# Performance work log

Hardware: AMD Instinct MI355X
Metric: run time of the kernel (lower is better)

## Reference

```python
import jax, jax.numpy as jnp
import numpy as np

# Dims (match init_kwargs / input_specs)
B, S, HID = 1, 2048, 2048
NH, NKV, HD = 16, 4, 128          # head_dim = HID // NH
REP = NH // NKV                    # num_key_value_groups
BLOCK_SIZE, LOCAL_BLOCKS, SINK_NUM = 8, 4, 4
SCALING = HD ** -0.5


def rotate_half(x):
    x1, x2 = jnp.split(x, 2, axis=-1)
    return jnp.concatenate([-x2, x1], axis=-1)


def setup_inputs() -> dict:
    key = jax.random.key(0)
    ks = jax.random.split(key, 7)
    return {
        "hidden_states": jax.random.normal(ks[0], (B, S, HID), jnp.float32),
        "cos": jax.random.uniform(ks[1], (B, S, HD), jnp.float32, minval=-1.0, maxval=1.0),
        "sin": jax.random.uniform(ks[2], (B, S, HD), jnp.float32, minval=-1.0, maxval=1.0),
        # Projection weights stored as [in, out] so x @ W matches nn.Linear (bias=False).
        "Wq": 0.02 * jax.random.normal(ks[3], (HID, NH * HD), jnp.float32),
        "Wk": 0.02 * jax.random.normal(ks[4], (HID, NKV * HD), jnp.float32),
        "Wv": 0.02 * jax.random.normal(ks[5], (HID, NKV * HD), jnp.float32),
        "Wo": 0.02 * jax.random.normal(ks[6], (NH * HD, HID), jnp.float32),
    }


def sink_local_mask(seq_len):
    # query i attends to: sink tokens j < min(SINK_NUM, i), and local window
    # max(0, i - LOCAL_BLOCKS*BLOCK_SIZE) <= j <= i (diagonal included so every
    # row has at least one valid key; see notes).
    i = jnp.arange(seq_len)[:, None]
    j = jnp.arange(seq_len)[None, :]
    sink = j < jnp.minimum(SINK_NUM, i)
    local = (j >= i - LOCAL_BLOCKS * BLOCK_SIZE) & (j <= i)
    return sink | local  # [S, S] bool, broadcast over (B, H)


def reference(hidden_states, cos, sin, Wq, Wk, Wv, Wo):
    # projections -> [B, H, S, D]
    q = (hidden_states @ Wq).reshape(B, S, NH, HD).transpose(0, 2, 1, 3)
    k = (hidden_states @ Wk).reshape(B, S, NKV, HD).transpose(0, 2, 1, 3)
    v = (hidden_states @ Wv).reshape(B, S, NKV, HD).transpose(0, 2, 1, 3)
    # rotary embedding, cos/sin broadcast over head dim (unsqueeze_dim=1)
    c = cos[:, None, :, :]
    s = sin[:, None, :, :]
    q = q * c + rotate_half(q) * s
    k = k * c + rotate_half(k) * s
    # repeat_kv (GQA) -> [B, NH, S, D]
    k = jnp.repeat(k, REP, axis=1)
    v = jnp.repeat(v, REP, axis=1)
    # sink + local sparse attention (dense compute + mask, as in source)
    scores = jnp.einsum('bhqd,bhkd->bhqk', q, k) * SCALING
    mask = sink_local_mask(S)
    scores = jnp.where(mask, scores, -jnp.inf)
    attn_weights = jax.nn.softmax(scores, axis=-1)
    attn_output = jnp.einsum('bhqk,bhkd->bhqd', attn_weights, v)
    # Faithful to source: view(B, S, -1) on the [B, H, S, D] layout WITHOUT a
    # transpose(1,2) first (the original code omits it).
    attn_output = attn_output.reshape(B, S, NH * HD)
    attn_output = attn_output @ Wo
    return attn_output, attn_weights
```

## Files before the change

kernel.cpp:

```cpp
#include <hip/hip_runtime.h>

typedef unsigned short ushort_t;
typedef __attribute__((ext_vector_type(8))) short short8;
typedef __attribute__((ext_vector_type(4))) float f32x4;
typedef __attribute__((ext_vector_type(8))) unsigned short us8;
typedef __attribute__((ext_vector_type(4))) unsigned short us4;

#define SEQ 2048
#define HIDD 2048
#define XLD 3072
#define SCALING 0.08838834764831843f

__device__ __forceinline__ float bf2f(ushort_t u) {
    unsigned int x = ((unsigned int)u) << 16;
    return __builtin_bit_cast(float, x);
}
__device__ __forceinline__ ushort_t f2bf(float f) {
    unsigned int u = __builtin_bit_cast(unsigned int, f);
    u += 0x7fffu + ((u >> 16) & 1u);
    return (ushort_t)(u >> 16);
}

__device__ __forceinline__ void transpose_tile(
    const float* __restrict__ W, ushort_t* __restrict__ Wt,
    int N, int n0, int k0, int dstRow0) {
    __shared__ ushort_t t[64 * 80];
    const int tid = threadIdx.x;
    {
        const int kl = tid >> 4;
        const int nc = (tid & 15) * 4;
        #pragma unroll
        for (int p = 0; p < 4; ++p) {
            int k = kl + p * 16;
            float4 v = *(const float4*)(W + (size_t)(k0 + k) * N + n0 + nc);
            t[(nc + 0) * 80 + k] = f2bf(v.x);
            t[(nc + 1) * 80 + k] = f2bf(v.y);
            t[(nc + 2) * 80 + k] = f2bf(v.z);
            t[(nc + 3) * 80 + k] = f2bf(v.w);
        }
    }
    __syncthreads();
    {
        const int nl = tid >> 3;
        const int kc = (tid & 7) * 8;
        #pragma unroll
        for (int p = 0; p < 2; ++p) {
            int n = nl + p * 32;
            *(us8*)(Wt + (size_t)(dstRow0 + n) * HIDD + k0 + kc) =
                *(const us8*)&t[n * 80 + kc];
        }
    }
}

__global__ __launch_bounds__(256) void transpose_all(
    const float* __restrict__ Wq, const float* __restrict__ Wk,
    const float* __restrict__ Wv, const float* __restrict__ Wo,
    const float* __restrict__ hid,
    ushort_t* __restrict__ Wqkvt, ushort_t* __restrict__ Wot,
    ushort_t* __restrict__ Hb) {
    int bx = blockIdx.x, k0 = blockIdx.y * 64;
    if (bx < 32)       transpose_tile(Wq, Wqkvt, 2048, bx * 64,        k0, bx * 64);
    else if (bx < 40)  transpose_tile(Wk, Wqkvt, 512,  (bx - 32) * 64, k0, 2048 + (bx - 32) * 64);
    else if (bx < 48)  transpose_tile(Wv, Wqkvt, 512,  (bx - 40) * 64, k0, 2560 + (bx - 40) * 64);
    else if (bx < 80)  transpose_tile(Wo, Wot,   2048, (bx - 48) * 64, k0, (bx - 48) * 64);
    else {
        int chunk = (bx - 80) * 32 + blockIdx.y;
        size_t base = (size_t)chunk * 4096 + threadIdx.x * 16;
        #pragma unroll
        for (int p = 0; p < 4; ++p) {
            float4 v = *(const float4*)(hid + base + p * 4);
            us4 o;
            o[0] = f2bf(v.x); o[1] = f2bf(v.y); o[2] = f2bf(v.z); o[3] = f2bf(v.w);
            *(us4*)(Hb + base + p * 4) = o;
        }
    }
}

__global__ __launch_bounds__(256) void gemm_splitk(
    const ushort_t* __restrict__ A, int lda,
    const ushort_t* __restrict__ Bt, int ldb,
    ushort_t* __restrict__ P, int ldc,
    const int4 kexts) {
    __shared__ ushort_t lA[2 * 128 * 32];
    __shared__ ushort_t lB[2 * 128 * 32];
    const int tid = threadIdx.x;
    const int wave = tid >> 6, lane = tid & 63;
    const int wm = wave >> 1, wn = wave & 1;
    const int quad = lane >> 4, l16 = lane & 15;
    const int m0 = blockIdx.y * 128, n0 = blockIdx.x * 128;
    const int z = blockIdx.z;

    const int ke[4] = {kexts.x, kexts.y, kexts.z, kexts.w};
    int koff = 0;
    for (int zz = 0; zz < 4; ++zz) if (zz < z) koff += ke[zz];
    const int kext = ke[z];

    A  += (size_t)koff;
    Bt += (size_t)koff;
    P  += (size_t)z * ((size_t)gridDim.y * 128) * ldc;

    const int srow = lane >> 2;
    const int scol = 8 * ((lane & 3) ^ (srow & 3));

    f32x4 acc[4][4] = {};

    const ushort_t* Ab = A  + (size_t)(m0 + wave * 16 + srow) * lda + scol;
    const ushort_t* Bb = Bt + (size_t)(n0 + wave * 16 + srow) * ldb + scol;
    ushort_t* lAw = lA + (wave * 16) * 32;
    ushort_t* lBw = lB + (wave * 16) * 32;

    const int rsw = (quad ^ (l16 & 3)) * 8;

    for (int kk = 0; kk < kext; kk += 64) {
        __syncthreads();
        #pragma unroll
        for (int kh = 0; kh < 2; ++kh) {
            #pragma unroll
            for (int c = 0; c < 2; ++c) {
                __builtin_amdgcn_global_load_lds(
                    (const __attribute__((address_space(1))) unsigned int*)(const void*)
                        (Ab + (size_t)(c * 64) * lda + kk + kh * 32),
                    (__attribute__((address_space(3))) unsigned int*)(void*)
                        (lAw + kh * 128 * 32 + c * 64 * 32), 16, 0, 0);
                __builtin_amdgcn_global_load_lds(
                    (const __attribute__((address_space(1))) unsigned int*)(const void*)
                        (Bb + (size_t)(c * 64) * ldb + kk + kh * 32),
                    (__attribute__((address_space(3))) unsigned int*)(void*)
                        (lBw + kh * 128 * 32 + c * 64 * 32), 16, 0, 0);
            }
        }
        __syncthreads();
        #pragma unroll
        for (int kh = 0; kh < 2; ++kh) {
            short8 af[4], bfr[4];
            #pragma unroll
            for (int mt = 0; mt < 4; ++mt)
                af[mt] = *(const short8*)&lA[kh * 128 * 32 + (wm * 64 + mt * 16 + l16) * 32 + rsw];
            #pragma unroll
            for (int nt = 0; nt < 4; ++nt)
                bfr[nt] = *(const short8*)&lB[kh * 128 * 32 + (wn * 64 + nt * 16 + l16) * 32 + rsw];
            #pragma unroll
            for (int mt = 0; mt < 4; ++mt) {
                #pragma unroll
                for (int nt = 0; nt < 4; ++nt)
                    acc[mt][nt] = __builtin_amdgcn_mfma_f32_16x16x32_bf16(
                        af[mt], bfr[nt], acc[mt][nt], 0, 0, 0);
            }
        }
    }

    #pragma unroll
    for (int mt = 0; mt < 4; ++mt) {
        #pragma unroll
        for (int nt = 0; nt < 4; ++nt) {
            int gm = m0 + wm * 64 + mt * 16 + quad * 4;
            int gn = n0 + wn * 64 + nt * 16 + l16;
            #pragma unroll
            for (int r = 0; r < 4; ++r)
                P[(size_t)(gm + r) * ldc + gn] = f2bf(acc[mt][nt][r]);
        }
    }
}

#define RWAVES (SEQ * 10)
#define VWAVES (SEQ * 2)
__global__ __launch_bounds__(256) void reduce_x(
    const ushort_t* __restrict__ P, ushort_t* __restrict__ X,
    const float* __restrict__ cosp, const float* __restrict__ sinp) {
    const size_t ZS = (size_t)SEQ * XLD;
    int wid = blockIdx.x * 4 + (threadIdx.x >> 6);
    int lane = threadIdx.x & 63;
    if (wid < RWAVES) {
        int s = wid / 10, seg = wid % 10;
        int c0 = seg * 256 + lane * 4;
        size_t base = (size_t)s * XLD + c0;
        us4 a = *(const us4*)(P + base);
        us4 b = *(const us4*)(P + ZS + base);
        float x[4];
        #pragma unroll
        for (int t = 0; t < 4; ++t) x[t] = bf2f(a[t]) + bf2f(b[t]);
        float p[4];
        #pragma unroll
        for (int t = 0; t < 4; ++t) p[t] = __shfl_xor(x[t], 16, 64);
        int d = (lane * 4) & 127;
        float4 cv = *(const float4*)(cosp + (size_t)s * 128 + d);
        float4 sv = *(const float4*)(sinp + (size_t)s * 128 + d);
        float sgn = (lane & 16) ? 1.f : -1.f;
        us4 o;
        o[0] = f2bf(x[0] * cv.x + sgn * p[0] * sv.x);
        o[1] = f2bf(x[1] * cv.y + sgn * p[1] * sv.y);
        o[2] = f2bf(x[2] * cv.z + sgn * p[2] * sv.z);
        o[3] = f2bf(x[3] * cv.w + sgn * p[3] * sv.w);
        *(us4*)(X + base) = o;
    } else {
        int w2 = wid - RWAVES;
        int s = w2 >> 1;
        int c0 = 2560 + (w2 & 1) * 256 + lane * 4;
        size_t base = (size_t)s * XLD + c0;
        us4 a = *(const us4*)(P + base);
        us4 b = *(const us4*)(P + ZS + base);
        us4 o;
        #pragma unroll
        for (int t = 0; t < 4; ++t) o[t] = f2bf(bf2f(a[t]) + bf2f(b[t]));
        *(us4*)(X + base) = o;
    }
}

__global__ __launch_bounds__(256) void reduce_out3(
    const ushort_t* __restrict__ P, float* __restrict__ out) {
    const size_t ZS = (size_t)SEQ * HIDD;
    size_t idx = ((size_t)blockIdx.x * 256 + threadIdx.x) * 4;
    us4 a = *(const us4*)(P + idx);
    us4 b = *(const us4*)(P + ZS + idx);
    us4 c = *(const us4*)(P + 2 * ZS + idx);
    float4 o;
    o.x = bf2f(a[0]) + bf2f(b[0]) + bf2f(c[0]);
    o.y = bf2f(a[1]) + bf2f(b[1]) + bf2f(c[1]);
    o.z = bf2f(a[2]) + bf2f(b[2]) + bf2f(c[2]);
    o.w = bf2f(a[3]) + bf2f(b[3]) + bf2f(c[3]);
    *(float4*)(out + idx) = o;
}

#define SMLD 136
__device__ __forceinline__ float qk_round_lds(
    const ushort_t* __restrict__ sm, const float* qf,
    int jg, int dg, int lo, int nsink, int w0, int r) {
    int jj = r * 16 + jg;
    int row;
    if (jj < nsink) row = 48 + jj;
    else {
        int widx = lo + jj - nsink - w0;
        if (widx > 47) widx = 47;
        row = widx;
    }
    const ushort_t* kp = sm + row * SMLD + dg * 32;
    float p = 0.f;
    #pragma unroll
    for (int pq = 0; pq < 4; ++pq) {
        us8 v = *(const us8*)(kp + pq * 8);
        #pragma unroll
        for (int t = 0; t < 8; ++t) p += qf[pq * 8 + t] * bf2f(v[t]);
    }
    p += __shfl_xor(p, 1, 64);
    p += __shfl_xor(p, 2, 64);
    return p * SCALING;
}

__global__ __launch_bounds__(256) void attn_kernel(
    const ushort_t* __restrict__ X, float* __restrict__ Wts,
    ushort_t* __restrict__ Aout) {
    __shared__ ushort_t sm[104 * SMLD];
    const int tid = threadIdx.x;
    const int lane = tid & 63;
    const int wv = tid >> 6;
    const int h = blockIdx.x >> 7;
    const int i0 = (blockIdx.x & 127) << 4;
    const int w0 = (i0 >= 32) ? (i0 - 32) : 0;
    const int kvh = h >> 2;

    const ushort_t* Kg = X + 2048 + kvh * 128;
    const ushort_t* Vg = X + 2560 + kvh * 128;

    #pragma unroll
    for (int p = 0; p < 7; ++p) {
        int tau = p * 16 + (tid >> 4);
        if (tau < 104) {
            int rr = (tau < 52) ? tau : (tau - 52);
            int grow = (rr < 48) ? (w0 + rr) : (rr - 48);
            const ushort_t* src = ((tau < 52) ? Kg : Vg) + (size_t)grow * XLD + (tid & 15) * 8;
            *(us8*)&sm[tau * SMLD + (tid & 15) * 8] = *(const us8*)src;
        }
    }
    __syncthreads();

    const int dg = lane & 3;
    const int jg = lane >> 2;

    for (int ii = 0; ii < 4; ++ii) {
        const int i = i0 + wv * 4 + ii;

        float qf[32];
        {
            const ushort_t* Q = X + (size_t)i * XLD + h * 128 + dg * 32;
            #pragma unroll
            for (int pq = 0; pq < 4; ++pq) {
                us8 v = *(const us8*)(Q + pq * 8);
                #pragma unroll
                for (int t = 0; t < 8; ++t) qf[pq * 8 + t] = bf2f(v[t]);
            }
        }

        int lo = i - 32; if (lo < 0) lo = 0;
        int nsink = lo < 4 ? lo : 4;
        int NJ = nsink + (i - lo + 1);

        float s0 = qk_round_lds(sm, qf, jg, dg, lo, nsink, w0, 0);
        float s1 = qk_round_lds(sm, qf, jg, dg, lo, nsink, w0, 1);
        float s2 = qk_round_lds(sm, qf, jg, dg, lo, nsink, w0, 2);

        int src = (lane & 15) * 4;
        float m0 = __shfl(s0, src, 64);
        float m1 = __shfl(s1, src, 64);
        float m2 = __shfl(s2, src, 64);
        float mysc = (lane < 16) ? m0 : ((lane < 32) ? m1 : m2);
        if (lane >= NJ) mysc = -1e30f;

        float m = mysc;
        #pragma unroll
        for (int off = 32; off > 0; off >>= 1) m = fmaxf(m, __shfl_xor(m, off, 64));

        float e = (lane < NJ) ? expf(mysc - m) : 0.f;
        float l = e;
        #pragma unroll
        for (int off = 32; off > 0; off >>= 1) l += __shfl_xor(l, off, 64);
        float w = e / l;

        float* row = Wts + ((size_t)h * SEQ + i) * SEQ;
        #pragma unroll
        for (int s = 0; s < 8; ++s) {
            float4 o;
            #pragma unroll
            for (int t = 0; t < 4; ++t) {
                int c = s * 256 + lane * 4 + t;
                bool in = (c < nsink) || (c >= lo && c <= i);
                int jjc = in ? ((c < nsink) ? c : (nsink + c - lo)) : 0;
                float wv2 = __shfl(w, jjc, 64);
                o[t] = in ? wv2 : 0.f;
            }
            *(float4*)(row + s * 256 + lane * 4) = o;
        }

        float o0 = 0.f, o1 = 0.f;
        for (int jj = 0; jj < NJ; ++jj) {
            int vrow;
            if (jj < nsink) vrow = 100 + jj;
            else {
                int widx = lo + jj - nsink - w0;
                vrow = 52 + widx;
            }
            float pb = __shfl(w, jj, 64);
            unsigned int vv = *(const unsigned int*)&sm[vrow * SMLD + 2 * lane];
            o0 += pb * bf2f((ushort_t)(vv & 0xffff));
            o1 += pb * bf2f((ushort_t)(vv >> 16));
        }
        int r = h * 128 + (i >> 4);
        int c = (i & 15) * 128 + 2 * lane;
        ushort_t* Ar = Aout + (size_t)r * HIDD + c;
        Ar[0] = f2bf(o0);
        Ar[1] = f2bf(o1);
    }
}

extern "C" void kernel_launch(void* const* d_in, const int* in_sizes, int n_in,
                              void* d_out, int out_size, void* d_ws, size_t ws_size,
                              hipStream_t stream) {
    if (n_in < 7) return;
    const float* hid  = (const float*)d_in[0];
    const float* cosp = (const float*)d_in[1];
    const float* sinp = (const float*)d_in[2];
    const float* Wq   = (const float*)d_in[3];
    const float* Wk   = (const float*)d_in[4];
    const float* Wv   = (const float*)d_in[5];
    const float* Wo   = (const float*)d_in[6];

    float* out = (float*)d_out;
    float* wts = out + (size_t)SEQ * HIDD;

    ushort_t* Hb    = (ushort_t*)d_ws;
    ushort_t* Wqkvt = Hb    + (size_t)2048 * 2048;
    ushort_t* Wot   = Wqkvt + (size_t)3072 * 2048;
    ushort_t* X     = Wot   + (size_t)2048 * 2048;
    ushort_t* Am    = X     + (size_t)SEQ * XLD;
    ushort_t* Pqkv  = Am    + (size_t)SEQ * HIDD;
    ushort_t* Pout  = Pqkv  + 2 * (size_t)SEQ * XLD;
    size_t need = ((char*)(Pout + 3 * (size_t)SEQ * HIDD)) - (char*)d_ws;
    if (ws_size < need) return;

    dim3 blk(256);
    transpose_all<<<dim3(112, 32), blk, 0, stream>>>(
        Wq, Wk, Wv, Wo, hid, Wqkvt, Wot, Hb);

    gemm_splitk<<<dim3(24, 16, 2), blk, 0, stream>>>(
        Hb, HIDD, Wqkvt, 2048, Pqkv, XLD, make_int4(1024, 1024, 0, 0));
    reduce_x<<<(RWAVES + VWAVES) / 4, blk, 0, stream>>>(
        Pqkv, X, cosp, sinp);

    attn_kernel<<<SEQ * 16 / 16, blk, 0, stream>>>(X, wts, Am);

    gemm_splitk<<<dim3(16, 16, 3), blk, 0, stream>>>(
        Am, HIDD, Wot, 2048, Pout, HIDD, make_int4(704, 704, 640, 0));
    reduce_out3<<<(SEQ * HIDD) / (256 * 4), blk, 0, stream>>>(Pout, out);
}
```

Before: 448.9 us.

## Swizzle attention LDS, use nontemporal stores, and coarsen reduce kernels

Three separate changes. The attention kernel's K/V shared-memory tile gets an XOR swizzle on 64-byte chunks to cut LDS bank conflicts in the QK and PV reads. The large attention-weights write and the final output write switch to nontemporal stores so they do not pollute the cache. The two reduce kernels each handle four work items per wave/thread with a quarter of the grid, to reduce launch and per-block overhead. The risks are swizzle indexing mistakes and lower memory-level parallelism from the smaller grids.

```diff
diff --git a/kernel.cpp b/kernel.cpp
--- a/kernel.cpp
+++ b/kernel.cpp
@@ -168,62 +168,70 @@
     const ushort_t* __restrict__ P, ushort_t* __restrict__ X,
     const float* __restrict__ cosp, const float* __restrict__ sinp) {
     const size_t ZS = (size_t)SEQ * XLD;
-    int wid = blockIdx.x * 4 + (threadIdx.x >> 6);
+    int wbase = (blockIdx.x * 4 + (threadIdx.x >> 6)) * 4;
     int lane = threadIdx.x & 63;
-    if (wid < RWAVES) {
-        int s = wid / 10, seg = wid % 10;
-        int c0 = seg * 256 + lane * 4;
-        size_t base = (size_t)s * XLD + c0;
-        us4 a = *(const us4*)(P + base);
-        us4 b = *(const us4*)(P + ZS + base);
-        float x[4];
-        #pragma unroll
-        for (int t = 0; t < 4; ++t) x[t] = bf2f(a[t]) + bf2f(b[t]);
-        float p[4];
-        #pragma unroll
-        for (int t = 0; t < 4; ++t) p[t] = __shfl_xor(x[t], 16, 64);
-        int d = (lane * 4) & 127;
-        float4 cv = *(const float4*)(cosp + (size_t)s * 128 + d);
-        float4 sv = *(const float4*)(sinp + (size_t)s * 128 + d);
-        float sgn = (lane & 16) ? 1.f : -1.f;
-        us4 o;
-        o[0] = f2bf(x[0] * cv.x + sgn * p[0] * sv.x);
-        o[1] = f2bf(x[1] * cv.y + sgn * p[1] * sv.y);
-        o[2] = f2bf(x[2] * cv.z + sgn * p[2] * sv.z);
-        o[3] = f2bf(x[3] * cv.w + sgn * p[3] * sv.w);
-        *(us4*)(X + base) = o;
-    } else {
-        int w2 = wid - RWAVES;
-        int s = w2 >> 1;
-        int c0 = 2560 + (w2 & 1) * 256 + lane * 4;
-        size_t base = (size_t)s * XLD + c0;
-        us4 a = *(const us4*)(P + base);
-        us4 b = *(const us4*)(P + ZS + base);
-        us4 o;
-        #pragma unroll
-        for (int t = 0; t < 4; ++t) o[t] = f2bf(bf2f(a[t]) + bf2f(b[t]));
-        *(us4*)(X + base) = o;
+    #pragma unroll
+    for (int pp = 0; pp < 4; ++pp) {
+        int wid = wbase + pp;
+        if (wid < RWAVES) {
+            int s = wid / 10, seg = wid % 10;
+            int c0 = seg * 256 + lane * 4;
+            size_t base = (size_t)s * XLD + c0;
+            us4 a = *(const us4*)(P + base);
+            us4 b = *(const us4*)(P + ZS + base);
+            float x[4];
+            #pragma unroll
+            for (int t = 0; t < 4; ++t) x[t] = bf2f(a[t]) + bf2f(b[t]);
+            float p[4];
+            #pragma unroll
+            for (int t = 0; t < 4; ++t) p[t] = __shfl_xor(x[t], 16, 64);
+            int d = (lane * 4) & 127;
+            float4 cv = *(const float4*)(cosp + (size_t)s * 128 + d);
+            float4 sv = *(const float4*)(sinp + (size_t)s * 128 + d);
+            float sgn = (lane & 16) ? 1.f : -1.f;
+            us4 o;
+            o[0] = f2bf(x[0] * cv.x + sgn * p[0] * sv.x);
+            o[1] = f2bf(x[1] * cv.y + sgn * p[1] * sv.y);
+            o[2] = f2bf(x[2] * cv.z + sgn * p[2] * sv.z);
+            o[3] = f2bf(x[3] * cv.w + sgn * p[3] * sv.w);
+            *(us4*)(X + base) = o;
+        } else {
+            int w2 = wid - RWAVES;
+            int s = w2 >> 1;
+            int c0 = 2560 + (w2 & 1) * 256 + lane * 4;
+            size_t base = (size_t)s * XLD + c0;
+            us4 a = *(const us4*)(P + base);
+            us4 b = *(const us4*)(P + ZS + base);
+            us4 o;
+            #pragma unroll
+            for (int t = 0; t < 4; ++t) o[t] = f2bf(bf2f(a[t]) + bf2f(b[t]));
+            *(us4*)(X + base) = o;
+        }
     }
 }
 
 __global__ __launch_bounds__(256) void reduce_out3(
     const ushort_t* __restrict__ P, float* __restrict__ out) {
     const size_t ZS = (size_t)SEQ * HIDD;
-    size_t idx = ((size_t)blockIdx.x * 256 + threadIdx.x) * 4;
-    us4 a = *(const us4*)(P + idx);
-    us4 b = *(const us4*)(P + ZS + idx);
-    us4 c = *(const us4*)(P + 2 * ZS + idx);
-    float4 o;
-    o.x = bf2f(a[0]) + bf2f(b[0]) + bf2f(c[0]);
-    o.y = bf2f(a[1]) + bf2f(b[1]) + bf2f(c[1]);
-    o.z = bf2f(a[2]) + bf2f(b[2]) + bf2f(c[2]);
-    o.w = bf2f(a[3]) + bf2f(b[3]) + bf2f(c[3]);
-    *(float4*)(out + idx) = o;
+    size_t idx0 = ((size_t)blockIdx.x * 256 + threadIdx.x) * 16;
+    #pragma unroll
+    for (int pp = 0; pp < 4; ++pp) {
+        size_t idx = idx0 + pp * 4;
+        us4 a = *(const us4*)(P + idx);
+        us4 b = *(const us4*)(P + ZS + idx);
+        us4 c = *(const us4*)(P + 2 * ZS + idx);
+        f32x4 o;
+        o[0] = bf2f(a[0]) + bf2f(b[0]) + bf2f(c[0]);
+        o[1] = bf2f(a[1]) + bf2f(b[1]) + bf2f(c[1]);
+        o[2] = bf2f(a[2]) + bf2f(b[2]) + bf2f(c[2]);
+        o[3] = bf2f(a[3]) + bf2f(b[3]) + bf2f(c[3]);
+        __builtin_nontemporal_store(o, (f32x4*)(out + idx));
+    }
 }
 
 #define SMLD 136
 __device__ __forceinline__ float qk_round_lds(
-    const ushort_t* __restrict__ sm, const float* qf,
+    const char* __restrict__ smb, const float* qf,
     int jg, int dg, int lo, int nsink, int w0, int r) {
     int jj = r * 16 + jg;
     int row;
@@ -233,11 +241,11 @@
         if (widx > 47) widx = 47;
         row = widx;
     }
-    const ushort_t* kp = sm + row * SMLD + dg * 32;
+    const char* base = smb + row * 272 + ((dg * 64) ^ ((row & 3) << 6));
     float p = 0.f;
     #pragma unroll
     for (int pq = 0; pq < 4; ++pq) {
-        us8 v = *(const us8*)(kp + pq * 8);
+        us8 v = *(const us8*)(base + pq * 16);
         #pragma unroll
         for (int t = 0; t < 8; ++t) p += qf[pq * 8 + t] * bf2f(v[t]);
     }
@@ -250,6 +258,7 @@
     const ushort_t* __restrict__ X, float* __restrict__ Wts,
     ushort_t* __restrict__ Aout) {
     __shared__ ushort_t sm[104 * SMLD];
+    char* smb = (char*)sm;
     const int tid = threadIdx.x;
     const int lane = tid & 63;
     const int wv = tid >> 6;
@@ -268,7 +277,8 @@
             int rr = (tau < 52) ? tau : (tau - 52);
             int grow = (rr < 48) ? (w0 + rr) : (rr - 48);
             const ushort_t* src = ((tau < 52) ? Kg : Vg) + (size_t)grow * XLD + (tid & 15) * 8;
-            *(us8*)&sm[tau * SMLD + (tid & 15) * 8] = *(const us8*)src;
+            int dst = tau * 272 + (((tid & 15) * 16) ^ ((tau & 3) << 6));
+            *(us8*)(smb + dst) = *(const us8*)src;
         }
     }
     __syncthreads();
@@ -294,9 +304,9 @@
         int nsink = lo < 4 ? lo : 4;
         int NJ = nsink + (i - lo + 1);
 
-        float s0 = qk_round_lds(sm, qf, jg, dg, lo, nsink, w0, 0);
-        float s1 = qk_round_lds(sm, qf, jg, dg, lo, nsink, w0, 1);
-        float s2 = qk_round_lds(sm, qf, jg, dg, lo, nsink, w0, 2);
+        float s0 = qk_round_lds(smb, qf, jg, dg, lo, nsink, w0, 0);
+        float s1 = qk_round_lds(smb, qf, jg, dg, lo, nsink, w0, 1);
+        float s2 = qk_round_lds(smb, qf, jg, dg, lo, nsink, w0, 2);
 
         int src = (lane & 15) * 4;
         float m0 = __shfl(s0, src, 64);
@@ -318,7 +328,7 @@
         float* row = Wts + ((size_t)h * SEQ + i) * SEQ;
         #pragma unroll
         for (int s = 0; s < 8; ++s) {
-            float4 o;
+            f32x4 o;
             #pragma unroll
             for (int t = 0; t < 4; ++t) {
                 int c = s * 256 + lane * 4 + t;
@@ -327,7 +337,7 @@
                 float wv2 = __shfl(w, jjc, 64);
                 o[t] = in ? wv2 : 0.f;
             }
-            *(float4*)(row + s * 256 + lane * 4) = o;
+            __builtin_nontemporal_store(o, (f32x4*)(row + s * 256 + lane * 4));
         }
 
         float o0 = 0.f, o1 = 0.f;
@@ -339,7 +349,8 @@
                 vrow = 52 + widx;
             }
             float pb = __shfl(w, jj, 64);
-            unsigned int vv = *(const unsigned int*)&sm[vrow * SMLD + 2 * lane];
+            unsigned int vv = *(const unsigned int*)
+                (smb + vrow * 272 + ((4 * lane) ^ ((vrow & 3) << 6)));
             o0 += pb * bf2f((ushort_t)(vv & 0xffff));
             o1 += pb * bf2f((ushort_t)(vv >> 16));
         }
@@ -382,12 +393,12 @@
 
     gemm_splitk<<<dim3(24, 16, 2), blk, 0, stream>>>(
         Hb, HIDD, Wqkvt, 2048, Pqkv, XLD, make_int4(1024, 1024, 0, 0));
-    reduce_x<<<(RWAVES + VWAVES) / 4, blk, 0, stream>>>(
+    reduce_x<<<(RWAVES + VWAVES) / 16, blk, 0, stream>>>(
         Pqkv, X, cosp, sinp);
 
     attn_kernel<<<SEQ * 16 / 16, blk, 0, stream>>>(X, wts, Am);
 
     gemm_splitk<<<dim3(16, 16, 3), blk, 0, stream>>>(
         Am, HIDD, Wot, 2048, Pout, HIDD, make_int4(704, 704, 640, 0));
-    reduce_out3<<<(SEQ * HIDD) / (256 * 4), blk, 0, stream>>>(Pout, out);
-}
+    reduce_out3<<<(SEQ * HIDD) / (256 * 16), blk, 0, stream>>>(Pout, out);
+}
```

Measured after the change: 450.5 us. Within noise of the previous version (+0.4%).
